# Kernel optimization log

Measured on AMD Instinct MI355X. Metric: run time of the kernel, lower is better.

## Reference

```python
import jax, jax.numpy as jnp
import numpy as np

B, L, G, N, K, E = 64, 512, 128, 32, 8, 65536
NTOK, D_TOK, H_DIR, NTL_INP, NHID, NREL = 10000, 64, 64, 32, 16, 16


def _bn(x, gamma, beta, eps=1e-5):
    # training-mode BatchNorm1d over axis 0; x: (n, C)
    mu = x.mean(0)
    var = x.var(0)
    return gamma * (x - mu) / jnp.sqrt(var + eps) + beta


def _lstm(x, w_ih, w_hh, b_ih, b_hh):
    # x: (B, T, D); torch gate order i, f, g, o
    nb = x.shape[0]
    H = w_hh.shape[1]
    def step(carry, xt):
        h, c = carry
        g = xt @ w_ih.T + b_ih + h @ w_hh.T + b_hh
        i, f, gg, o = jnp.split(g, 4, axis=-1)
        c = jax.nn.sigmoid(f) * c + jax.nn.sigmoid(i) * jnp.tanh(gg)
        h = jax.nn.sigmoid(o) * jnp.tanh(c)
        return (h, c), h
    init = (jnp.zeros((nb, H), x.dtype), jnp.zeros((nb, H), x.dtype))
    _, hs = jax.lax.scan(step, init, jnp.swapaxes(x, 0, 1))
    return jnp.swapaxes(hs, 0, 1)


def setup_inputs() -> dict:
    key = jax.random.key(0)
    ks = jax.random.split(key, 24)
    inp = {}
    inp['seq'] = jax.random.randint(ks[0], (B, L), 0, NTOK)
    inp['pos2grp'] = jax.random.randint(ks[1], (B, L), 0, G)
    inp['idx'] = jax.random.randint(ks[2], (B, N, K), 0, L)
    inp['u'] = jax.random.randint(ks[3], (E,), 0, B * N)
    inp['v'] = jax.random.randint(ks[4], (E,), 0, B * N)
    # parameters
    s = 1.0 / np.sqrt(H_DIR)
    inp['tok_emb'] = jax.random.normal(ks[5], (NTOK, D_TOK), jnp.float32)
    for tag, k0 in (('f', 6), ('b', 10)):
        inp[f'w_ih_{tag}'] = s * jax.random.normal(ks[k0], (4 * H_DIR, D_TOK), jnp.float32)
        inp[f'w_hh_{tag}'] = s * jax.random.normal(ks[k0 + 1], (4 * H_DIR, H_DIR), jnp.float32)
        inp[f'b_ih_{tag}'] = s * jax.random.normal(ks[k0 + 2], (4 * H_DIR,), jnp.float32)
        inp[f'b_hh_{tag}'] = s * jax.random.normal(ks[k0 + 3], (4 * H_DIR,), jnp.float32)
    inp['w_src'] = (1.0 / np.sqrt(2 * H_DIR)) * jax.random.normal(ks[14], (NTL_INP, 2 * H_DIR), jnp.float32)
    inp['b_src'] = jnp.zeros((NTL_INP,), jnp.float32)
    inp['w_dst'] = (1.0 / np.sqrt(2 * H_DIR)) * jax.random.normal(ks[15], (NTL_INP, 2 * H_DIR), jnp.float32)
    inp['b_dst'] = jnp.zeros((NTL_INP,), jnp.float32)
    inp['g_src'] = jnp.ones((NTL_INP,), jnp.float32)
    inp['be_src'] = jnp.zeros((NTL_INP,), jnp.float32)
    inp['g_dst'] = jnp.ones((NTL_INP,), jnp.float32)
    inp['be_dst'] = jnp.zeros((NTL_INP,), jnp.float32)
    inp['ntl_w'] = 0.001 * jax.random.normal(ks[16], (NREL, NHID, NTL_INP, NTL_INP), jnp.float32)
    inp['ntl_v'] = 0.001 * jax.random.normal(ks[17], (NREL, NHID, 2 * NTL_INP), jnp.float32)
    inp['ntl_b'] = jnp.zeros((NREL, NHID, 1), jnp.float32)
    inp['ntl_u'] = 0.001 * jax.random.normal(ks[18], (NREL, 1, NHID), jnp.float32)
    inp['ntl_g'] = jnp.ones((NREL * NHID,), jnp.float32)
    inp['ntl_be'] = jnp.zeros((NREL * NHID,), jnp.float32)
    return inp


def reference(seq, pos2grp, idx, u, v, tok_emb,
              w_ih_f, w_hh_f, b_ih_f, b_hh_f,
              w_ih_b, w_hh_b, b_ih_b, b_hh_b,
              w_src, b_src, w_dst, b_dst,
              g_src, be_src, g_dst, be_dst,
              ntl_w, ntl_v, ntl_b, ntl_u, ntl_g, ntl_be):
    # token embed + scatter-sum tokens -> groups
    x_tok = tok_emb[seq]                                   # (B, L, D)
    gid = (pos2grp + jnp.arange(B)[:, None] * G).reshape(-1)
    x_grp = jax.ops.segment_sum(x_tok.reshape(B * L, -1), gid,
                                num_segments=B * G).reshape(B, G, -1)
    # bidirectional LSTM over groups
    hf = _lstm(x_grp, w_ih_f, w_hh_f, b_ih_f, b_hh_f)
    hb = jnp.flip(_lstm(jnp.flip(x_grp, 1), w_ih_b, w_hh_b, b_ih_b, b_hh_b), 1)
    h_grp = jnp.concatenate([hf, hb], -1)                  # (B, G, 2H)
    # hierarchical gather + sum: node <- sum over K token positions' groups
    b_idx = jnp.arange(B)[:, None, None]
    g_idx = pos2grp[b_idx, idx]                            # (B, N, K)
    h = h_grp[b_idx, g_idx].sum(2).reshape(B * N, -1)      # (B*N, 2H)
    # edge endpoint projections + batchnorm
    hs = _bn(h[u] @ w_src.T + b_src, g_src, be_src)        # (E, ninp)
    ht = _bn(h[v] @ w_dst.T + b_dst, g_dst, be_dst)
    # Neural Tensor Layer
    linear = jnp.einsum('rhd,nd->rhn', ntl_v, jnp.concatenate([hs, ht], 1))
    bil = jnp.stack([
        jnp.einsum('nhj,nj->hn', jnp.einsum('ni,hij->nhj', hs, ntl_w[r]), ht)
        for r in range(NREL)], 0)                          # (R, H, E)
    z = bil + linear + ntl_b
    mu = z.mean(-1, keepdims=True)
    var = z.var(-1, keepdims=True)
    zn = ntl_g.reshape(NREL, NHID, 1) * (z - mu) / jnp.sqrt(var + 1e-5) \
         + ntl_be.reshape(NREL, NHID, 1)
    t = jnp.tanh(zn)
    logit = jnp.einsum('rh,rhn->nr', ntl_u[:, 0, :], t)    # (E, R)
    return logit
```

## Files before the change

kernel.cpp:

```cpp
#include <hip/hip_runtime.h>
#include <hip/hip_bf16.h>
#include <hip/hip_fp16.h>
#include <cstdint>

constexpr int B_   = 64;
constexpr int L_   = 512;
constexpr int G_   = 128;
constexpr int E_   = 65536;
constexpr int RH   = 256;
constexpr int M_   = 2048;
constexpr int JA   = 33;
constexpr int COLS = RH * JA;
constexpr int NREP = 16;

typedef _Float16 v2h __attribute__((ext_vector_type(2)));
typedef _Float16 v8h __attribute__((ext_vector_type(8)));
typedef float    v4f __attribute__((ext_vector_type(4)));
typedef union { uint4 u4; v8h h8; } cvt8;

#define DEV static __device__ __forceinline__

DEV float sigm(float x) { return 1.f / (1.f + __expf(-x)); }
DEV float tanh_fast(float x) {
    x = fminf(15.f, fmaxf(-15.f, x));
    float e = __expf(2.f * x);
    return (e - 1.f) / (e + 1.f);
}

__global__ __launch_bounds__(256) void k_eh(const int* __restrict__ seq,
                                            const int* __restrict__ p2g,
                                            const float* __restrict__ emb,
                                            const int* __restrict__ u,
                                            const int* __restrict__ v,
                                            const float* __restrict__ ntlw,
                                            const float* __restrict__ ntlv,
                                            const float* __restrict__ ntlb,
                                            float* __restrict__ xg,
                                            int* __restrict__ cu, int* __restrict__ cv,
                                            float* __restrict__ waug) {
    int blk = blockIdx.x;
    int t   = threadIdx.x;
    if (blk >= 512) {
        int gid = (blk - 512) * 256 + t;
        int i   = gid / COLS;
        int rem = gid - i * COLS;
        int rh  = rem / JA;
        int j   = rem - rh * JA;
        float val;
        if (i < 32) val = (j < 32) ? ntlw[((size_t)rh * 32 + i) * 32 + j] : ntlv[rh * 64 + i];
        else        val = (j < 32) ? ntlv[rh * 64 + 32 + j] : ntlb[rh];
        waug[(size_t)i * COLS + j * 256 + rh] = val;
        return;
    }
    if (blk >= 256) {
        int n = (blk - 256) * 256 + t;
        atomicAdd(&cu[u[n]], 1);
        atomicAdd(&cv[v[n]], 1);
        return;
    }
    __shared__ float xgl[G_ * 64];
    __shared__ int sl[128], gld[128];
    int b = blk >> 2, part = blk & 3;
    for (int i = t; i < G_ * 64; i += 256) xgl[i] = 0.f;
    if (t < 128) {
        sl[t]  = seq[b * L_ + part * 128 + t];
        gld[t] = p2g[b * L_ + part * 128 + t];
    }
    __syncthreads();
    int d = t & 63, sub = t >> 6;
#pragma unroll
    for (int gg = 0; gg < 2; gg++) {
        int sv[16], gv[16];
#pragma unroll
        for (int k = 0; k < 16; k++) {
            sv[k] = sl[sub * 32 + gg * 16 + k];
            gv[k] = gld[sub * 32 + gg * 16 + k];
        }
#pragma unroll
        for (int k = 0; k < 16; k++)
            atomicAdd(&xgl[gv[k] * 64 + d], emb[(size_t)sv[k] * 64 + d]);
    }
    __syncthreads();
    for (int i = t; i < G_ * 64; i += 256)
        atomicAdd(&xg[(size_t)b * G_ * 64 + i], xgl[i]);
}

__global__ __launch_bounds__(256) void k_pre(const float* __restrict__ xg,
                                             const float* __restrict__ wihf,
                                             const float* __restrict__ bihf,
                                             const float* __restrict__ bhhf,
                                             const float* __restrict__ wihb,
                                             const float* __restrict__ bihb,
                                             const float* __restrict__ bhhb,
                                             float* __restrict__ pre,
                                             const int* __restrict__ cu,
                                             int* __restrict__ ustart,
                                             int* __restrict__ ucursor) {
    int blk = blockIdx.x;
    int t   = threadIdx.x;
    if (blk == 512) {
        __shared__ int ps[256];
        int base = t * 8, run = 0;
        int c[8], loc[8];
#pragma unroll
        for (int i = 0; i < 8; i++) c[i] = cu[base + i];
#pragma unroll
        for (int i = 0; i < 8; i++) { loc[i] = run; run += c[i]; }
        ps[t] = run;
        __syncthreads();
        for (int off = 1; off < 256; off <<= 1) {
            int a = (t >= off) ? ps[t - off] : 0;
            __syncthreads();
            ps[t] += a;
            __syncthreads();
        }
        int ex = ps[t] - run;
#pragma unroll
        for (int i = 0; i < 8; i++) { ustart[base + i] = ex + loc[i]; ucursor[base + i] = ex + loc[i]; }
        if (t == 255) ustart[2048] = E_;
        return;
    }
    int dir = blk >> 8;
    const float* wih = dir ? wihb : wihf;
    float bias = dir ? (bihb[t] + bhhb[t]) : (bihf[t] + bhhf[t]);
    int r0 = (blk & 255) * 32;

    float4 wv[16];
#pragma unroll
    for (int c = 0; c < 16; c++) wv[c] = ((const float4*)(wih + t * 64))[c];

#pragma unroll 2
    for (int ml = 0; ml < 32; ml++) {
        const float* xr = xg + (size_t)(r0 + ml) * 64;
        float acc = bias;
#pragma unroll
        for (int c = 0; c < 16; c++) {
            float x0 = xr[4 * c], x1 = xr[4 * c + 1], x2 = xr[4 * c + 2], x3 = xr[4 * c + 3];
            acc += x0 * wv[c].x + x1 * wv[c].y + x2 * wv[c].z + x3 * wv[c].w;
        }
        pre[((size_t)dir * 8192 + r0 + ml) * 256 + t] = acc;
    }
}

__global__ __launch_bounds__(256, 1) void k_lstm(const float* __restrict__ pre,
                                                 const float* __restrict__ whh_f,
                                                 const float* __restrict__ whh_b,
                                                 float* __restrict__ hgrp,
                                                 const int* __restrict__ u,
                                                 const int* __restrict__ v,
                                                 int* __restrict__ ucursor,
                                                 int2* __restrict__ eonv) {
    int blk = blockIdx.x;
    int t   = threadIdx.x;
    if (blk >= 128) {
        int n = (blk - 128) * 256 + t;
        int pos = atomicAdd(&ucursor[u[n]], 1);
        eonv[pos] = make_int2(n, v[n]);
        return;
    }
    __shared__ __align__(16) float plds[64][256];
    __shared__ __align__(16) float hist[64][64];
    __shared__ float gl[2][256];
    int dir = blk >> 6;
    int b   = blk & 63;
    const float* whh = dir ? whh_b : whh_f;
    const float* src = pre + ((size_t)dir * 8192 + (size_t)b * G_) * 256;
    int e = t & 63;
    int q = t >> 6;

    float4 wv[16];
#pragma unroll
    for (int c = 0; c < 16; c++) wv[c] = ((const float4*)(whh + (size_t)t * 64))[c];

    float h = 0.f, creg = 0.f;

    for (int half = 0; half < 2; half++) {
        {
            int base = (dir ^ half) ? 64 : 0;
            const float4* s4 = (const float4*)(src + (size_t)base * 256);
            float4* d4 = (float4*)&plds[0][0];
#pragma unroll
            for (int i = 0; i < 16; i++) d4[i * 256 + t] = s4[i * 256 + t];
        }
        __syncthreads();
        for (int kk = 0; kk < 64; kk++) {
            int k = half * 64 + kk;
            int srow = dir ? (63 - kk) : kk;
            float p = plds[srow][t];
            float a0 = p, a1 = 0.f, a2 = 0.f, a3 = 0.f;
#pragma unroll
            for (int c = 0; c < 16; c++) {
                float f0 = __int_as_float(__builtin_amdgcn_readlane(__float_as_int(h), 4 * c + 0));
                float f1 = __int_as_float(__builtin_amdgcn_readlane(__float_as_int(h), 4 * c + 1));
                float f2 = __int_as_float(__builtin_amdgcn_readlane(__float_as_int(h), 4 * c + 2));
                float f3 = __int_as_float(__builtin_amdgcn_readlane(__float_as_int(h), 4 * c + 3));
                a0 += wv[c].x * f0;
                a1 += wv[c].y * f1;
                a2 += wv[c].z * f2;
                a3 += wv[c].w * f3;
            }
            float g = (a0 + a1) + (a2 + a3);
            gl[k & 1][t] = (q == 2) ? tanh_fast(g) : sigm(g);
            __syncthreads();
            float ai = gl[k & 1][e];
            float af = gl[k & 1][64 + e];
            float ag = gl[k & 1][128 + e];
            float ao = gl[k & 1][192 + e];
            creg = af * creg + ai * ag;
            h = ao * tanh_fast(creg);
            if (q == 0) hist[srow][e] = h;
        }
        __syncthreads();
        int sbase = (dir ? (1 - half) : half) * 64;
#pragma unroll
        for (int i = 0; i < 16; i++) {
            int row = q * 16 + i;
            int s = sbase + row;
            hgrp[((size_t)(b * G_ + s)) * 128 + dir * 64 + e] = hist[row][e];
        }
    }
}

__global__ __launch_bounds__(256) void k_gp(const int* __restrict__ idx,
                                            const int* __restrict__ p2g,
                                            const float* __restrict__ hgrp,
                                            const int* __restrict__ cu,
                                            const int* __restrict__ cv,
                                            const float* __restrict__ wsrc,
                                            const float* __restrict__ bsrc,
                                            const float* __restrict__ wdst,
                                            const float* __restrict__ bdst,
                                            float* __restrict__ Ps, float* __restrict__ Pd,
                                            float* __restrict__ bn_raw) {
    __shared__ __align__(16) float hsl[8][128];
    __shared__ float red[256];
    int m0 = blockIdx.x * 8;
    int t  = threadIdx.x;
    int d = t & 127, mh = t >> 7;
#pragma unroll
    for (int rep = 0; rep < 4; rep++) {
        int ml = rep * 2 + mh;
        int m  = m0 + ml;
        int b  = m >> 5;
        float acc = 0.f;
#pragma unroll
        for (int k = 0; k < 8; k++) {
            int l = idx[m * 8 + k];
            int g = p2g[b * L_ + l];
            acc += hgrp[((size_t)b * G_ + g) * 128 + d];
        }
        hsl[ml][d] = acc;
    }
    __syncthreads();
    int ml = t >> 5, o = t & 31;
    int m  = m0 + ml;
    const float4* hp = (const float4*)&hsl[ml][0];
    float cw_u = (float)cu[m], cw_v = (float)cv[m];
#pragma unroll 1
    for (int side = 0; side < 2; side++) {
        const float* W = side ? wdst : wsrc;
        float4 wr[32];
#pragma unroll
        for (int c = 0; c < 32; c++) wr[c] = ((const float4*)(W + (size_t)o * 128))[c];
        float acc = side ? bdst[o] : bsrc[o];
#pragma unroll
        for (int c = 0; c < 32; c++) {
            float4 h4 = hp[c];
            acc += h4.x * wr[c].x + h4.y * wr[c].y + h4.z * wr[c].z + h4.w * wr[c].w;
        }
        (side ? Pd : Ps)[(size_t)m * 32 + o] = acc;
        float cw = side ? cw_v : cw_u;
        red[t] = cw * acc;
        __syncthreads();
        if (t < 32) {
            float s = 0.f;
#pragma unroll
            for (int i = 0; i < 8; i++) s += red[i * 32 + t];
            atomicAdd(&bn_raw[side * 64 + t], s);
        }
        __syncthreads();
        red[t] = cw * acc * acc;
        __syncthreads();
        if (t < 32) {
            float s = 0.f;
#pragma unroll
            for (int i = 0; i < 8; i++) s += red[i * 32 + t];
            atomicAdd(&bn_raw[side * 64 + 32 + t], s);
        }
        __syncthreads();
    }
}

__global__ __launch_bounds__(256) void k_prep(const float* __restrict__ Ps,
                                              const float* __restrict__ Pd,
                                              const float* __restrict__ bn_raw,
                                              const float* __restrict__ gs,
                                              const float* __restrict__ bes,
                                              const float* __restrict__ gd,
                                              const float* __restrict__ bed,
                                              float* __restrict__ hsaugT,
                                              v2h* __restrict__ htp) {
    int blk = blockIdx.x;
    int t   = threadIdx.x;
    constexpr float invE = 1.f / (float)E_;
    if (blk < 264) {
        int gid = blk * 256 + t;
        int c = gid >> 11;
        int m = gid & 2047;
        float val = 1.f;
        if (c < 32) {
            float mu  = bn_raw[c] * invE;
            float isd = rsqrtf(bn_raw[32 + c] * invE - mu * mu + 1e-5f);
            val = gs[c] * (Ps[(size_t)m * 32 + c] - mu) * isd + bes[c];
        }
        hsaugT[(size_t)c * 2048 + m] = val;
        return;
    }
    int gid = (blk - 264) * 256 + t;
    int m  = gid >> 4;
    int jp = gid & 15;
    int j0 = 2 * jp, j1 = 2 * jp + 1;
    float mu0  = bn_raw[64 + j0] * invE;
    float isd0 = rsqrtf(bn_raw[96 + j0] * invE - mu0 * mu0 + 1e-5f);
    float mu1  = bn_raw[64 + j1] * invE;
    float isd1 = rsqrtf(bn_raw[96 + j1] * invE - mu1 * mu1 + 1e-5f);
    float h0 = gd[j0] * (Pd[(size_t)m * 32 + j0] - mu0) * isd0 + bed[j0];
    float h1 = gd[j1] * (Pd[(size_t)m * 32 + j1] - mu1) * isd1 + bed[j1];
    v2h p;
    p.x = (_Float16)h0; p.y = (_Float16)h1;
    htp[gid] = p;
}

__global__ __launch_bounds__(256, 1) void k_agemm(const float* __restrict__ hsaugT,
                                                  const float* __restrict__ waug,
                                                  v2h* __restrict__ Ah,
                                                  float* __restrict__ A32) {
    int ms = blockIdx.x;
    int jp = blockIdx.y;
    int t  = threadIdx.x;
    int mbase = ms * 128;
    if (jp < 16) {
        float w0[JA], w1[JA];
#pragma unroll
        for (int i = 0; i < JA; i++) {
            w0[i] = waug[(size_t)i * COLS + (2 * jp) * 256 + t];
            w1[i] = waug[(size_t)i * COLS + (2 * jp + 1) * 256 + t];
        }
#pragma unroll 1
        for (int ch = 0; ch < 16; ch++) {
            int m0 = mbase + ch * 8;
            float acc0[8], acc1[8];
#pragma unroll
            for (int ml = 0; ml < 8; ml++) { acc0[ml] = 0.f; acc1[ml] = 0.f; }
#pragma unroll
            for (int i = 0; i < JA; i++) {
                const float* hr = hsaugT + (size_t)i * 2048 + m0;
#pragma unroll
                for (int ml = 0; ml < 8; ml++) {
                    float hv = hr[ml];
                    acc0[ml] += hv * w0[i];
                    acc1[ml] += hv * w1[i];
                }
            }
#pragma unroll
            for (int ml = 0; ml < 8; ml++) {
                v2h p;
                p.x = (_Float16)acc0[ml]; p.y = (_Float16)acc1[ml];
                Ah[(size_t)(m0 + ml) * 4096 + jp * 256 + t] = p;
            }
        }
    } else {
        float w2[JA];
#pragma unroll
        for (int i = 0; i < JA; i++) w2[i] = waug[(size_t)i * COLS + 32 * 256 + t];
#pragma unroll 1
        for (int ch = 0; ch < 16; ch++) {
            int m0 = mbase + ch * 8;
            float acc[8];
#pragma unroll
            for (int ml = 0; ml < 8; ml++) acc[ml] = 0.f;
#pragma unroll
            for (int i = 0; i < JA; i++) {
                const float* hr = hsaugT + (size_t)i * 2048 + m0;
#pragma unroll
                for (int ml = 0; ml < 8; ml++) acc[ml] += hr[ml] * w2[i];
            }
#pragma unroll
            for (int ml = 0; ml < 8; ml++)
                A32[(size_t)(m0 + ml) * 256 + t] = acc[ml];
        }
    }
}

__global__ __launch_bounds__(256) void k_z(const unsigned int* __restrict__ Ah,
                                           const float* __restrict__ A32,
                                           const uint4* __restrict__ htp4,
                                           const int* __restrict__ ustart,
                                           const int2* __restrict__ eonv,
                                           _Float16* __restrict__ zh,
                                           float* __restrict__ zsumR,
                                           float* __restrict__ zsqR) {
    int t    = threadIdx.x;
    int lane = t & 63;
    int uu   = blockIdx.x * 4 + (t >> 6);
    int l15  = lane & 15, quad = lane >> 4;

    uint4 bf[16];
#pragma unroll
    for (int nt = 0; nt < 16; nt++) {
        const unsigned int* bp = Ah + (size_t)uu * 4096 + (quad * 4) * 256 + nt * 16 + l15;
        bf[nt].x = bp[0]; bf[nt].y = bp[256]; bf[nt].z = bp[512]; bf[nt].w = bp[768];
    }
    float a32[16];
#pragma unroll
    for (int nt = 0; nt < 16; nt++) a32[nt] = A32[(size_t)uu * 256 + nt * 16 + l15];

    float s1[16], s2[16];
#pragma unroll
    for (int nt = 0; nt < 16; nt++) { s1[nt] = 0.f; s2[nt] = 0.f; }

    int e0 = ustart[uu], e1 = ustart[uu + 1];
    for (int base = e0; base < e1; base += 16) {
        int ei = min(base + l15, e1 - 1);
        int2 q = eonv[ei];
        uint4 afu = htp4[(size_t)q.y * 4 + quad];
        cvt8 ac; ac.u4 = afu;
        int nrow[4], valid[4];
#pragma unroll
        for (int r = 0; r < 4; r++) {
            int er = quad * 4 + r;
            nrow[r]  = __builtin_amdgcn_ds_bpermute(er << 2, q.x);
            valid[r] = (base + er) < e1;
        }
#pragma unroll
        for (int nt = 0; nt < 16; nt++) {
            cvt8 bc; bc.u4 = bf[nt];
            v4f acc = { a32[nt], a32[nt], a32[nt], a32[nt] };
            acc = __builtin_amdgcn_mfma_f32_16x16x32_f16(ac.h8, bc.h8, acc, 0, 0, 0);
#pragma unroll
            for (int r = 0; r < 4; r++) {
                if (valid[r]) {
                    float z = acc[r];
                    zh[(size_t)nrow[r] * 256 + nt * 16 + l15] = (_Float16)z;
                    s1[nt] += z; s2[nt] += z * z;
                }
            }
        }
    }
    int rep = (blockIdx.x & (NREP - 1)) * 256;
#pragma unroll
    for (int nt = 0; nt < 16; nt++) {
        float a = s1[nt], b = s2[nt];
        a += __shfl_xor(a, 16); a += __shfl_xor(a, 32);
        b += __shfl_xor(b, 16); b += __shfl_xor(b, 32);
        if (quad == 0) {
            atomicAdd(&zsumR[rep + nt * 16 + l15], a);
            atomicAdd(&zsqR[rep + nt * 16 + l15], b);
        }
    }
}

__global__ __launch_bounds__(256) void k_logit(const _Float16* __restrict__ zh,
                                               const float* __restrict__ zsumR,
                                               const float* __restrict__ zsqR,
                                               const float* __restrict__ ntlu,
                                               const float* __restrict__ ntlg,
                                               const float* __restrict__ ntlbe,
                                               float* __restrict__ out) {
    int t  = threadIdx.x;
    int n0 = blockIdx.x * 16;
    float su = 0.f, sq = 0.f;
#pragma unroll
    for (int r = 0; r < NREP; r++) {
        su += zsumR[r * 256 + t];
        sq += zsqR[r * 256 + t];
    }
    float mu  = su / (float)E_;
    float var = sq / (float)E_ - mu * mu;
    float isd = rsqrtf(var + 1e-5f);
    float g   = ntlg[t],  be  = ntlbe[t];
    float uw  = ntlu[t];
    float zv[16];
#pragma unroll
    for (int nl = 0; nl < 16; nl++)
        zv[nl] = (float)zh[(size_t)(n0 + nl) * 256 + t];
#pragma unroll 1
    for (int nl = 0; nl < 16; nl++) {
        float zn  = g * (zv[nl] - mu) * isd + be;
        float val = uw * tanh_fast(zn);
        val += __shfl_xor(val, 1);
        val += __shfl_xor(val, 2);
        val += __shfl_xor(val, 4);
        val += __shfl_xor(val, 8);
        if ((t & 15) == 0) out[(size_t)(n0 + nl) * 16 + (t >> 4)] = val;
    }
}

extern "C" void kernel_launch(void* const* d_in, const int* in_sizes, int n_in,
                              void* d_out, int out_size, void* d_ws, size_t ws_size,
                              hipStream_t stream) {
    const int*   seq   = (const int*)d_in[0];
    const int*   p2g   = (const int*)d_in[1];
    const int*   idx   = (const int*)d_in[2];
    const int*   u     = (const int*)d_in[3];
    const int*   v     = (const int*)d_in[4];
    const float* emb   = (const float*)d_in[5];
    const float* wihf  = (const float*)d_in[6];
    const float* whhf  = (const float*)d_in[7];
    const float* bihf  = (const float*)d_in[8];
    const float* bhhf  = (const float*)d_in[9];
    const float* wihb  = (const float*)d_in[10];
    const float* whhb  = (const float*)d_in[11];
    const float* bihb  = (const float*)d_in[12];
    const float* bhhb  = (const float*)d_in[13];
    const float* wsrc  = (const float*)d_in[14];
    const float* bsrc  = (const float*)d_in[15];
    const float* wdst  = (const float*)d_in[16];
    const float* bdst  = (const float*)d_in[17];
    const float* gs    = (const float*)d_in[18];
    const float* bes   = (const float*)d_in[19];
    const float* gd    = (const float*)d_in[20];
    const float* bed   = (const float*)d_in[21];
    const float* ntlw  = (const float*)d_in[22];
    const float* ntlv  = (const float*)d_in[23];
    const float* ntlb  = (const float*)d_in[24];
    const float* ntlu  = (const float*)d_in[25];
    const float* ntlg  = (const float*)d_in[26];
    const float* ntlbe = (const float*)d_in[27];
    float* out = (float*)d_out;

    char* ws = (char*)d_ws;
    size_t off = 0;
    auto take = [&](size_t bytes) -> char* {
        char* p = ws + off;
        off = (off + bytes + 255) & ~(size_t)255;
        return p;
    };
    int*   cnt_u  = (int*)  take(2048 * 4);
    int*   cnt_v  = (int*)  take(2048 * 4);
    float* zsumR  = (float*)take((size_t)NREP * 256 * 4);
    float* zsqR   = (float*)take((size_t)NREP * 256 * 4);
    float* bn_raw = (float*)take(128 * 4);
    float* x_grp  = (float*)take((size_t)B_ * G_ * 64 * 4);
    size_t zero_bytes = off;
    int*   ucursor = (int*)  take(2048 * 4);
    int*   ustart  = (int*)  take(2049 * 4);
    int2*  eonv    = (int2*) take((size_t)E_ * 8);
    float* pre     = (float*)take((size_t)2 * 8192 * 256 * 4);
    float* hgrp    = (float*)take((size_t)B_ * G_ * 128 * 4);
    float* Psrc    = (float*)take((size_t)M_ * 32 * 4);
    float* Pdst    = (float*)take((size_t)M_ * 32 * 4);
    float* hsaugT  = (float*)take((size_t)36 * 2048 * 4);
    v2h*   htp     = (v2h*)  take((size_t)M_ * 16 * 4);
    float* waug    = (float*)take((size_t)JA * COLS * 4);
    v2h*   Ah      = (v2h*)  take((size_t)M_ * 4096 * 4);
    float* A32     = (float*)take((size_t)M_ * 256 * 4);
    _Float16* zbuf = (_Float16*)take((size_t)E_ * 256 * 2);
    (void)ws_size; (void)in_sizes; (void)n_in; (void)out_size;

    hipMemsetAsync(d_ws, 0, zero_bytes, stream);

    k_eh<<<512 + 1089, 256, 0, stream>>>(seq, p2g, emb, u, v, ntlw, ntlv, ntlb,
                                         x_grp, cnt_u, cnt_v, waug);
    k_pre<<<513, 256, 0, stream>>>(x_grp, wihf, bihf, bhhf, wihb, bihb, bhhb, pre,
                                   cnt_u, ustart, ucursor);
    k_lstm<<<384, 256, 0, stream>>>(pre, whhf, whhb, hgrp, u, v, ucursor, eonv);
    k_gp<<<M_ / 8, 256, 0, stream>>>(idx, p2g, hgrp, cnt_u, cnt_v,
                                     wsrc, bsrc, wdst, bdst, Psrc, Pdst, bn_raw);
    k_prep<<<392, 256, 0, stream>>>(Psrc, Pdst, bn_raw, gs, bes, gd, bed, hsaugT, htp);
    k_agemm<<<dim3(16, 17), 256, 0, stream>>>(hsaugT, waug, Ah, A32);
    k_z<<<512, 256, 0, stream>>>((const unsigned int*)Ah, A32, (const uint4*)htp,
                                 ustart, eonv, zbuf, zsumR, zsqR);
    k_logit<<<E_ / 16, 256, 0, stream>>>(zbuf, zsumR, zsqR, ntlu, ntlg, ntlbe, out);
}
```

Baseline: 351.8 us.

## Run each LSTM direction in a single wave with packed FMA gates

The recurrent LSTM kernel now runs one 64-thread wavefront per (batch, direction). Each lane computes all four gates for its hidden unit, holding W_hh in registers as packed float2 pairs and broadcasting h via readlane. This removes the per-step __syncthreads and LDS gate exchange. The pre-activations are prefetched one step ahead straight from global memory instead of being staged in LDS, and the edge-bucketing tail is relaunched with 64-thread blocks. In exchange, each lane holds 256 weight floats, which raises register pressure and risks spills, and each lane does four times the serial FMA work per step.

```diff
diff --git a/kernel.cpp b/kernel.cpp
--- a/kernel.cpp
+++ b/kernel.cpp
@@ -16,6 +16,7 @@
 typedef _Float16 v2h __attribute__((ext_vector_type(2)));
 typedef _Float16 v8h __attribute__((ext_vector_type(8)));
 typedef float    v4f __attribute__((ext_vector_type(4)));
+typedef float    v2f32 __attribute__((ext_vector_type(2)));
 typedef union { uint4 u4; v8h h8; } cvt8;
 
 #define DEV static __device__ __forceinline__
@@ -142,82 +143,80 @@
     }
 }
 
-__global__ __launch_bounds__(256, 1) void k_lstm(const float* __restrict__ pre,
-                                                 const float* __restrict__ whh_f,
-                                                 const float* __restrict__ whh_b,
-                                                 float* __restrict__ hgrp,
-                                                 const int* __restrict__ u,
-                                                 const int* __restrict__ v,
-                                                 int* __restrict__ ucursor,
-                                                 int2* __restrict__ eonv) {
+__global__ __launch_bounds__(64, 1) void k_lstm(const float* __restrict__ pre,
+                                                const float* __restrict__ whh_f,
+                                                const float* __restrict__ whh_b,
+                                                float* __restrict__ hgrp,
+                                                const int* __restrict__ u,
+                                                const int* __restrict__ v,
+                                                int* __restrict__ ucursor,
+                                                int2* __restrict__ eonv) {
     int blk = blockIdx.x;
-    int t   = threadIdx.x;
+    int e   = threadIdx.x;
     if (blk >= 128) {
-        int n = (blk - 128) * 256 + t;
+        int n = (blk - 128) * 64 + e;
         int pos = atomicAdd(&ucursor[u[n]], 1);
         eonv[pos] = make_int2(n, v[n]);
         return;
     }
-    __shared__ __align__(16) float plds[64][256];
-    __shared__ __align__(16) float hist[64][64];
-    __shared__ float gl[2][256];
     int dir = blk >> 6;
     int b   = blk & 63;
-    const float* whh = dir ? whh_b : whh_f;
-    const float* src = pre + ((size_t)dir * 8192 + (size_t)b * G_) * 256;
-    int e = t & 63;
-    int q = t >> 6;
-
-    float4 wv[16];
-#pragma unroll
-    for (int c = 0; c < 16; c++) wv[c] = ((const float4*)(whh + (size_t)t * 64))[c];
+    const float* whh     = dir ? whh_b : whh_f;
+    const float* prebase = pre + ((size_t)dir * 8192 + (size_t)b * G_) * 256;
+    float* hout = hgrp + (size_t)b * G_ * 128 + dir * 64 + e;
+
+    v2f32 w01[64], w23[64];
+    {
+        const float4* pi = (const float4*)(whh + (size_t)(0 * 64 + e) * 64);
+        const float4* pf = (const float4*)(whh + (size_t)(1 * 64 + e) * 64);
+        const float4* pg = (const float4*)(whh + (size_t)(2 * 64 + e) * 64);
+        const float4* po = (const float4*)(whh + (size_t)(3 * 64 + e) * 64);
+#pragma unroll
+        for (int c = 0; c < 16; c++) {
+            float4 a = pi[c], f = pf[c], g = pg[c], o = po[c];
+            w01[4 * c + 0] = (v2f32){a.x, f.x};
+            w01[4 * c + 1] = (v2f32){a.y, f.y};
+            w01[4 * c + 2] = (v2f32){a.z, f.z};
+            w01[4 * c + 3] = (v2f32){a.w, f.w};
+            w23[4 * c + 0] = (v2f32){g.x, o.x};
+            w23[4 * c + 1] = (v2f32){g.y, o.y};
+            w23[4 * c + 2] = (v2f32){g.z, o.z};
+            w23[4 * c + 3] = (v2f32){g.w, o.w};
+        }
+    }
 
     float h = 0.f, creg = 0.f;
-
-    for (int half = 0; half < 2; half++) {
+    int sfirst = dir ? (G_ - 1) : 0;
+    float p0 = prebase[(size_t)sfirst * 256 + e];
+    float p1 = prebase[(size_t)sfirst * 256 + 64 + e];
+    float p2 = prebase[(size_t)sfirst * 256 + 128 + e];
+    float p3 = prebase[(size_t)sfirst * 256 + 192 + e];
+
+#pragma unroll 1
+    for (int step = 0; step < G_; step++) {
+        int s  = dir ? (G_ - 1 - step) : step;
+        int sn = dir ? (s - 1 < 0 ? 0 : s - 1) : (s + 1 > G_ - 1 ? G_ - 1 : s + 1);
+        float q0 = p0, q1 = p1, q2 = p2, q3 = p3;
         {
-            int base = (dir ^ half) ? 64 : 0;
-            const float4* s4 = (const float4*)(src + (size_t)base * 256);
-            float4* d4 = (float4*)&plds[0][0];
-#pragma unroll
-            for (int i = 0; i < 16; i++) d4[i * 256 + t] = s4[i * 256 + t];
-        }
-        __syncthreads();
-        for (int kk = 0; kk < 64; kk++) {
-            int k = half * 64 + kk;
-            int srow = dir ? (63 - kk) : kk;
-            float p = plds[srow][t];
-            float a0 = p, a1 = 0.f, a2 = 0.f, a3 = 0.f;
-#pragma unroll
-            for (int c = 0; c < 16; c++) {
-                float f0 = __int_as_float(__builtin_amdgcn_readlane(__float_as_int(h), 4 * c + 0));
-                float f1 = __int_as_float(__builtin_amdgcn_readlane(__float_as_int(h), 4 * c + 1));
-                float f2 = __int_as_float(__builtin_amdgcn_readlane(__float_as_int(h), 4 * c + 2));
-                float f3 = __int_as_float(__builtin_amdgcn_readlane(__float_as_int(h), 4 * c + 3));
-                a0 += wv[c].x * f0;
-                a1 += wv[c].y * f1;
-                a2 += wv[c].z * f2;
-                a3 += wv[c].w * f3;
-            }
-            float g = (a0 + a1) + (a2 + a3);
-            gl[k & 1][t] = (q == 2) ? tanh_fast(g) : sigm(g);
-            __syncthreads();
-            float ai = gl[k & 1][e];
-            float af = gl[k & 1][64 + e];
-            float ag = gl[k & 1][128 + e];
-            float ao = gl[k & 1][192 + e];
-            creg = af * creg + ai * ag;
-            h = ao * tanh_fast(creg);
-            if (q == 0) hist[srow][e] = h;
-        }
-        __syncthreads();
-        int sbase = (dir ? (1 - half) : half) * 64;
-#pragma unroll
-        for (int i = 0; i < 16; i++) {
-            int row = q * 16 + i;
-            int s = sbase + row;
-            hgrp[((size_t)(b * G_ + s)) * 128 + dir * 64 + e] = hist[row][e];
-        }
+            const float* pn = prebase + (size_t)sn * 256;
+            p0 = pn[e]; p1 = pn[64 + e]; p2 = pn[128 + e]; p3 = pn[192 + e];
+        }
+        v2f32 a01 = {q0, q1};
+        v2f32 a23 = {q2, q3};
+#pragma unroll
+        for (int j = 0; j < 64; j++) {
+            float hv = __int_as_float(__builtin_amdgcn_readlane(__float_as_int(h), j));
+            v2f32 hv2 = {hv, hv};
+            a01 += w01[j] * hv2;
+            a23 += w23[j] * hv2;
+        }
+        float ai = sigm(a01.x);
+        float af = sigm(a01.y);
+        float ag = tanh_fast(a23.x);
+        float ao = sigm(a23.y);
+        creg = af * creg + ai * ag;
+        h    = ao * tanh_fast(creg);
+        hout[(size_t)s * 128] = h;
     }
 }
 
@@ -564,7 +563,7 @@
                                          x_grp, cnt_u, cnt_v, waug);
     k_pre<<<513, 256, 0, stream>>>(x_grp, wihf, bihf, bhhf, wihb, bihb, bhhb, pre,
                                    cnt_u, ustart, ucursor);
-    k_lstm<<<384, 256, 0, stream>>>(pre, whhf, whhb, hgrp, u, v, ucursor, eonv);
+    k_lstm<<<128 + E_ / 64, 64, 0, stream>>>(pre, whhf, whhb, hgrp, u, v, ucursor, eonv);
     k_gp<<<M_ / 8, 256, 0, stream>>>(idx, p2g, hgrp, cnt_u, cnt_v,
                                      wsrc, bsrc, wdst, bdst, Psrc, Pdst, bn_raw);
     k_prep<<<392, 256, 0, stream>>>(Psrc, Pdst, bn_raw, gs, bes, gd, bed, hsaugT, htp);
```

After: 445.3 us. 1.27x slower.

## Stream LSTM preactivations with register prefetch instead of LDS staging

Applied to the files above, without the earlier changes.

The LSTM recurrence kernel no longer stages 64-step chunks of preactivations and hidden history in shared memory. Each step instead loads its preactivation from global memory two steps ahead into a rotating register pipeline, and writes h straight to global memory. This removes the bulk chunk copies, the extra barriers and about 80KB of LDS per block. In exchange, every step of the serial recurrence now issues a global load and store, whose latency must be hidden by the prefetch distance.

```diff
diff --git a/kernel.cpp b/kernel.cpp
--- a/kernel.cpp
+++ b/kernel.cpp
@@ -158,66 +158,57 @@
         eonv[pos] = make_int2(n, v[n]);
         return;
     }
-    __shared__ __align__(16) float plds[64][256];
-    __shared__ __align__(16) float hist[64][64];
     __shared__ float gl[2][256];
+    int q   = t >> 6;
+    int e   = t & 63;
     int dir = blk >> 6;
     int b   = blk & 63;
-    const float* whh = dir ? whh_b : whh_f;
-    const float* src = pre + ((size_t)dir * 8192 + (size_t)b * G_) * 256;
-    int e = t & 63;
-    int q = t >> 6;
+    const float* whh     = dir ? whh_b : whh_f;
+    const float* prebase = pre + ((size_t)dir * 8192 + (size_t)b * G_) * 256;
 
     float4 wv[16];
 #pragma unroll
-    for (int c = 0; c < 16; c++) wv[c] = ((const float4*)(whh + (size_t)t * 64))[c];
+    for (int c = 0; c < 16; c++) wv[c] = ((const float4*)(whh + t * 64))[c];
 
     float h = 0.f, creg = 0.f;
 
-    for (int half = 0; half < 2; half++) {
-        {
-            int base = (dir ^ half) ? 64 : 0;
-            const float4* s4 = (const float4*)(src + (size_t)base * 256);
-            float4* d4 = (float4*)&plds[0][0];
-#pragma unroll
-            for (int i = 0; i < 16; i++) d4[i * 256 + t] = s4[i * 256 + t];
-        }
+    int s0i = dir ? (G_ - 1) : 0;
+    int s1i = dir ? (G_ - 2) : 1;
+    float pq = prebase[(size_t)s0i * 256 + t];
+    float pr = prebase[(size_t)s1i * 256 + t];
+
+#pragma unroll 1
+    for (int step = 0; step < G_; step++) {
+        int s  = dir ? (G_ - 1 - step) : step;
+        int t2 = (step + 2 < G_) ? step + 2 : G_ - 1;
+        int s2 = dir ? (G_ - 1 - t2) : t2;
+        float pn = prebase[(size_t)s2 * 256 + t];
+
+        float a0 = pq, a1 = 0.f, a2 = 0.f, a3 = 0.f;
+#pragma unroll
+        for (int c = 0; c < 16; c++) {
+            float f0 = __int_as_float(__builtin_amdgcn_readlane(__float_as_int(h), 4 * c + 0));
+            float f1 = __int_as_float(__builtin_amdgcn_readlane(__float_as_int(h), 4 * c + 1));
+            float f2 = __int_as_float(__builtin_amdgcn_readlane(__float_as_int(h), 4 * c + 2));
+            float f3 = __int_as_float(__builtin_amdgcn_readlane(__float_as_int(h), 4 * c + 3));
+            a0 += wv[c].x * f0;
+            a1 += wv[c].y * f1;
+            a2 += wv[c].z * f2;
+            a3 += wv[c].w * f3;
+        }
+        float g = (a0 + a1) + (a2 + a3);
+        gl[step & 1][t] = (q == 2) ? tanh_fast(g) : sigm(g);
         __syncthreads();
-        for (int kk = 0; kk < 64; kk++) {
-            int k = half * 64 + kk;
-            int srow = dir ? (63 - kk) : kk;
-            float p = plds[srow][t];
-            float a0 = p, a1 = 0.f, a2 = 0.f, a3 = 0.f;
-#pragma unroll
-            for (int c = 0; c < 16; c++) {
-                float f0 = __int_as_float(__builtin_amdgcn_readlane(__float_as_int(h), 4 * c + 0));
-                float f1 = __int_as_float(__builtin_amdgcn_readlane(__float_as_int(h), 4 * c + 1));
-                float f2 = __int_as_float(__builtin_amdgcn_readlane(__float_as_int(h), 4 * c + 2));
-                float f3 = __int_as_float(__builtin_amdgcn_readlane(__float_as_int(h), 4 * c + 3));
-                a0 += wv[c].x * f0;
-                a1 += wv[c].y * f1;
-                a2 += wv[c].z * f2;
-                a3 += wv[c].w * f3;
-            }
-            float g = (a0 + a1) + (a2 + a3);
-            gl[k & 1][t] = (q == 2) ? tanh_fast(g) : sigm(g);
-            __syncthreads();
-            float ai = gl[k & 1][e];
-            float af = gl[k & 1][64 + e];
-            float ag = gl[k & 1][128 + e];
-            float ao = gl[k & 1][192 + e];
-            creg = af * creg + ai * ag;
-            h = ao * tanh_fast(creg);
-            if (q == 0) hist[srow][e] = h;
-        }
-        __syncthreads();
-        int sbase = (dir ? (1 - half) : half) * 64;
-#pragma unroll
-        for (int i = 0; i < 16; i++) {
-            int row = q * 16 + i;
-            int s = sbase + row;
-            hgrp[((size_t)(b * G_ + s)) * 128 + dir * 64 + e] = hist[row][e];
-        }
+        float ai = gl[step & 1][e];
+        float af = gl[step & 1][64 + e];
+        float ag = gl[step & 1][128 + e];
+        float ao = gl[step & 1][192 + e];
+        creg = af * creg + ai * ag;
+        h    = ao * tanh_fast(creg);
+        if (q == 0)
+            hgrp[((size_t)(b * G_ + s)) * 128 + dir * 64 + e] = h;
+
+        pq = pr; pr = pn;
     }
 }
 
```

Measured after the change: 360.5 us. 2.5% more time.
